# Optimization experiments

Hardware: AMD Instinct MI355X
Metric: run time of the kernel (lower is better)

The kernel has to match this reference:

```python
import jax, jax.numpy as jnp
import numpy as np

TEMPERATURE = 10.0
CE_WEIGHT = 10.0
NUM_CLUSTERS = 32  # clusters per batch element, labels in [0, K)


def setup_inputs() -> dict:
    key = jax.random.key(0)
    k1, k2, k3, k4, k5 = jax.random.split(key, 5)
    B, N, D, C, K = 4, 2048, 2, 64, NUM_CLUSTERS
    embedding = jax.random.normal(k1, (B, N, D), dtype=jnp.float32)
    contr_emb = jax.random.normal(k2, (B, N, C), dtype=jnp.float32)
    abs_coords = jax.random.normal(k3, (B, N, D), dtype=jnp.float32)
    patch_mask = jax.random.randint(k4, (B, N, N), 0, 2, dtype=jnp.int32)
    cluster_labels = jax.random.randint(k5, (B, N), 0, K, dtype=jnp.int32)
    return {
        "embedding": embedding,
        "contr_emb": contr_emb,
        "abs_coords": abs_coords,
        "patch_mask": patch_mask,
        "cluster_labels": cluster_labels,
    }


def reference(embedding, contr_emb, abs_coords, patch_mask, cluster_labels):
    B, N, D = embedding.shape
    C = contr_emb.shape[-1]
    K = NUM_CLUSTERS

    # --- anchor term: pairwise distance + nonlinearity + masked mean ---
    # diff[b,i,j,:] = (e_i - e_j) + (c_i - c_j)
    diff = (embedding[:, :, None] - embedding[:, None]) + (
        abs_coords[:, :, None] - abs_coords[:, None]
    )  # [B,N,N,D]
    dist_sq = jnp.sum(diff * diff, axis=-1)  # norm(2)^2, [B,N,N]
    nonlinear_dist = 1.0 - jnp.exp(-dist_sq / TEMPERATURE)
    m = (patch_mask == 1).astype(nonlinear_dist.dtype)
    loss = jnp.sum(nonlinear_dist * m) / jnp.sum(m)  # masked mean

    # --- contrastive term ---
    # F.normalize(contr_emb, dim=-1)
    norm = jnp.maximum(jnp.linalg.norm(contr_emb, axis=-1, keepdims=True), 1e-12)
    c = contr_emb / norm  # [B,N,C]

    # per-batch cluster means under no_grad (stop_gradient)
    onehot = jax.nn.one_hot(cluster_labels, K, dtype=c.dtype)  # [B,N,K]
    sums = jnp.einsum("bnc,bnk->bkc", c, onehot)  # [B,K,C]
    counts = jnp.maximum(jnp.sum(onehot, axis=1), 1.0)  # [B,K]
    means = jax.lax.stop_gradient(sums / counts[..., None])  # [B,K,C]

    # cat per-batch [C,K] matrices along cluster axis -> [C, B*K]
    cum_mean_clusters = means.reshape(B * K, C).T
    stacked = c.reshape(B * N, C)
    logits = stacked @ cum_mean_clusters  # [B*N, B*K]

    target = cluster_labels.reshape(-1)  # labels as written (no batch offset)
    logp = jax.nn.log_softmax(logits, axis=-1)
    nll = -jnp.take_along_axis(logp, target[:, None].astype(jnp.int32), axis=1)[:, 0]
    bce_loss = jnp.mean(nll)  # all targets >= 0, so no ignore_index hits

    return loss + CE_WEIGHT * bce_loss
```

## Files before the change

kernel.cpp:

```cpp
#include <hip/hip_runtime.h>
#include <math.h>

#define B_ 4
#define N_ 2048
#define C_ 64
#define K_ 32
#define BN_ (B_ * N_)

#define WS_NLL 0
#define WS_DONE 8
#define WS_MEANS 64
#define WS_APART 8320

__device__ __forceinline__ void pair4(float sx, float sy, float4 xs, float4 ys,
                                      int4 m, float& acc, int& cnt) {
  float dx, dy, d2, v;
  dx = sx - xs.x; dy = sy - ys.x; d2 = dx * dx + dy * dy;
  v = 1.0f - __expf(d2 * -0.1f);
  if (m.x == 1) { acc += v; cnt += 1; }
  dx = sx - xs.y; dy = sy - ys.y; d2 = dx * dx + dy * dy;
  v = 1.0f - __expf(d2 * -0.1f);
  if (m.y == 1) { acc += v; cnt += 1; }
  dx = sx - xs.z; dy = sy - ys.z; d2 = dx * dx + dy * dy;
  v = 1.0f - __expf(d2 * -0.1f);
  if (m.z == 1) { acc += v; cnt += 1; }
  dx = sx - xs.w; dy = sy - ys.w; d2 = dx * dx + dy * dy;
  v = 1.0f - __expf(d2 * -0.1f);
  if (m.w == 1) { acc += v; cnt += 1; }
}

__global__ __launch_bounds__(256) void k_main(
    const float* __restrict__ emb, const float* __restrict__ absc,
    const float* __restrict__ contr, const int* __restrict__ labels,
    const int* __restrict__ mask, float* __restrict__ ws) {
  __shared__ union {
    struct { float sx[N_]; float sy[N_]; } a;
    struct { int lab[N_]; float lsum[4][64]; float lcnt[4]; } c;
  } sm;
  __shared__ float red[8];
  int t = threadIdx.x, lane = t & 63, w = t >> 6;
  int bid = blockIdx.x;
  if (bid < 128) {
    int b = bid >> 5, k = bid & 31;
    if (bid == 0 && t == 0) {
      ws[WS_NLL] = 0.0f;
      ((unsigned*)ws)[WS_DONE] = 0u;
    }
    const int4* lab4 = (const int4*)(labels + b * N_);
    int4* l4 = (int4*)sm.c.lab;
    l4[t] = lab4[t];
    l4[t + 256] = lab4[t + 256];
    __syncthreads();
    float acc = 0.0f, cnt = 0.0f;
    for (int g0 = w * 512; g0 < w * 512 + 512; g0 += 64) {
      unsigned long long mb = __ballot(sm.c.lab[g0 + lane] == k);
      while (mb) {
        int bit = __ffsll(mb) - 1;
        mb &= mb - 1;
        int r = g0 + bit;
        float x = contr[(size_t)(b * N_ + r) * C_ + lane];
        float ss = x * x;
#pragma unroll
        for (int off = 32; off > 0; off >>= 1) ss += __shfl_xor(ss, off);
        acc += x * (1.0f / fmaxf(sqrtf(ss), 1e-12f));
        cnt += 1.0f;
      }
    }
    sm.c.lsum[w][lane] = acc;
    if (lane == 0) sm.c.lcnt[w] = cnt;
    __syncthreads();
    if (t < 64) {
      float s = sm.c.lsum[0][t] + sm.c.lsum[1][t] + sm.c.lsum[2][t] + sm.c.lsum[3][t];
      float c = sm.c.lcnt[0] + sm.c.lcnt[1] + sm.c.lcnt[2] + sm.c.lcnt[3];
      ws[WS_MEANS + (b * K_ + k) * C_ + t] = s / fmaxf(c, 1.0f);
    }
  } else {
    int aid = bid - 128;
    int b = aid >> 8;
    int flat = (aid & 255) * 256 + t;
    const float4* e4 = (const float4*)(emb + b * N_ * 2);
    const float4* a4 = (const float4*)(absc + b * N_ * 2);
    for (int i = t; i < N_ / 2; i += 256) {
      float4 ev = e4[i], av = a4[i];
      sm.a.sx[2 * i]     = ev.x + av.x;
      sm.a.sy[2 * i]     = ev.y + av.y;
      sm.a.sx[2 * i + 1] = ev.z + av.z;
      sm.a.sy[2 * i + 1] = ev.w + av.w;
    }
    __syncthreads();
    int cg = flat & 511;
    float4 xs = ((const float4*)sm.a.sx)[cg];
    float4 ys = ((const float4*)sm.a.sy)[cg];
    const int4* m4 = (const int4*)mask + (size_t)b * (N_ * (size_t)N_ / 4);
    float acc = 0.0f;
    int cnt = 0;
#pragma unroll
    for (int it = 0; it < 16; ++it) {
      int idx = flat + it * 65536;
      int4 m = m4[idx];
      int row = idx >> 9;
      pair4(sm.a.sx[row], sm.a.sy[row], xs, ys, m, acc, cnt);
    }
    float cntf = (float)cnt;
#pragma unroll
    for (int off = 32; off > 0; off >>= 1) {
      acc += __shfl_xor(acc, off);
      cntf += __shfl_xor(cntf, off);
    }
    if (lane == 0) { red[w * 2] = acc; red[w * 2 + 1] = cntf; }
    __syncthreads();
    if (t == 0) {
      ws[WS_APART + aid * 2 + 0] = red[0] + red[2] + red[4] + red[6];
      ws[WS_APART + aid * 2 + 1] = red[1] + red[3] + red[5] + red[7];
    }
  }
}

__global__ __launch_bounds__(128) void k_logits_final(
    const float* __restrict__ contr, const int* __restrict__ labels,
    float* __restrict__ ws, float* __restrict__ out) {
  __shared__ float lc[32 * C_];
  __shared__ float invr[32];
  __shared__ float lm[2][32], lsv[2][32], ltl[32];
  __shared__ float fred[4];
  __shared__ int lastf;
  int t = threadIdx.x, lane = t & 63, w = t >> 6;
  int r0 = blockIdx.x * 32;
  int j = w * 64 + lane;
  const float4* mean4 = (const float4*)(ws + WS_MEANS);
  float4 mk[16];
#pragma unroll
  for (int q = 0; q < 16; ++q) mk[q] = mean4[j * 16 + q];
  const float4* c4 = (const float4*)(contr + (size_t)r0 * C_);
  float4* lc4 = (float4*)lc;
  lc4[t] = c4[t];
  lc4[t + 128] = c4[t + 128];
  lc4[t + 256] = c4[t + 256];
  lc4[t + 384] = c4[t + 384];
  __syncthreads();
  for (int r = w * 16; r < w * 16 + 16; ++r) {
    float x = lc[r * C_ + lane];
    float ss = x * x;
#pragma unroll
    for (int off = 32; off > 0; off >>= 1) ss += __shfl_xor(ss, off);
    if (lane == 0) invr[r] = 1.0f / fmaxf(sqrtf(ss), 1e-12f);
  }
  __syncthreads();
  for (int r = 0; r < 32; ++r) {
    const float4* cr = lc4 + r * 16;
    float acc = 0.0f;
#pragma unroll
    for (int q = 0; q < 16; ++q) {
      float4 cv = cr[q];
      acc += cv.x * mk[q].x + cv.y * mk[q].y + cv.z * mk[q].z + cv.w * mk[q].w;
    }
    acc *= invr[r];
    float m = acc;
#pragma unroll
    for (int off = 32; off > 0; off >>= 1) m = fmaxf(m, __shfl_xor(m, off));
    float s = __expf(acc - m);
#pragma unroll
    for (int off = 32; off > 0; off >>= 1) s += __shfl_xor(s, off);
    int tgt = labels[r0 + r];
    float tl = __shfl(acc, tgt);
    if (lane == 0) {
      lm[w][r] = m;
      lsv[w][r] = s;
      if (w == 0) ltl[r] = tl;
    }
  }
  __syncthreads();
  if (t < 32) {
    float m0 = lm[0][t], m1 = lm[1][t];
    float mm = fmaxf(m0, m1);
    float ss = lsv[0][t] * __expf(m0 - mm) + lsv[1][t] * __expf(m1 - mm);
    float nll = (mm + __logf(ss)) - ltl[t];
#pragma unroll
    for (int off = 16; off > 0; off >>= 1) nll += __shfl_xor(nll, off);
    if (t == 0) atomicAdd(&ws[WS_NLL], nll);
  }
  __syncthreads();
  if (t == 0) {
    __threadfence();
    unsigned v = atomicAdd(&((unsigned*)ws)[WS_DONE], 1u);
    lastf = (v == 255u);
  }
  __syncthreads();
  if (lastf) {
    __threadfence();
    float a = 0.0f, c = 0.0f;
    for (int i = t; i < 1024; i += 128) {
      a += ws[WS_APART + i * 2 + 0];
      c += ws[WS_APART + i * 2 + 1];
    }
#pragma unroll
    for (int off = 32; off > 0; off >>= 1) {
      a += __shfl_xor(a, off);
      c += __shfl_xor(c, off);
    }
    if (lane == 0) { fred[w * 2] = a; fred[w * 2 + 1] = c; }
    __syncthreads();
    if (t == 0) {
      float at = fred[0] + fred[2];
      float ct = fred[1] + fred[3];
      out[0] = at / ct + 10.0f * ws[WS_NLL] * (1.0f / (float)BN_);
    }
  }
}

extern "C" void kernel_launch(void* const* d_in, const int* in_sizes, int n_in,
                              void* d_out, int out_size, void* d_ws, size_t ws_size,
                              hipStream_t stream) {
  const float* emb    = (const float*)d_in[0];
  const float* contr  = (const float*)d_in[1];
  const float* absc   = (const float*)d_in[2];
  const int*   mask   = (const int*)d_in[3];
  const int*   labels = (const int*)d_in[4];
  float* ws  = (float*)d_ws;
  float* out = (float*)d_out;

  k_main<<<128 + 1024, 256, 0, stream>>>(emb, absc, contr, labels, mask, ws);
  k_logits_final<<<256, 128, 0, stream>>>(contr, labels, ws, out);
}
```

Baseline: 154.8 us.

## Drop max-subtraction in softmax, halve rows per block, batch dot products

The logits kernel now handles 16 rows per block across 512 blocks instead of 32 rows across 256. The softmax max reduction is removed, which is safe because the logits are cosine-like values with magnitude at most about 1. The 16 dot products are computed first and their shuffle reductions run afterwards, and each row norm is computed by a single thread instead of a wave shuffle. This shortens the serial dependency chain and spreads the work over more blocks. In exchange, each block reloads the mean vectors, so twice as much mean data is read in total.

```diff
diff --git a/kernel.cpp b/kernel.cpp
--- a/kernel.cpp
+++ b/kernel.cpp
@@ -119,13 +119,13 @@
 __global__ __launch_bounds__(128) void k_logits_final(
     const float* __restrict__ contr, const int* __restrict__ labels,
     float* __restrict__ ws, float* __restrict__ out) {
-  __shared__ float lc[32 * C_];
-  __shared__ float invr[32];
-  __shared__ float lm[2][32], lsv[2][32], ltl[32];
+  __shared__ float lc[16 * C_];
+  __shared__ float invr[16];
+  __shared__ float lsv[2][16], ltl[16];
   __shared__ float fred[4];
   __shared__ int lastf;
   int t = threadIdx.x, lane = t & 63, w = t >> 6;
-  int r0 = blockIdx.x * 32;
+  int r0 = blockIdx.x * 16;
   int j = w * 64 + lane;
   const float4* mean4 = (const float4*)(ws + WS_MEANS);
   float4 mk[16];
@@ -135,55 +135,54 @@
   float4* lc4 = (float4*)lc;
   lc4[t] = c4[t];
   lc4[t + 128] = c4[t + 128];
-  lc4[t + 256] = c4[t + 256];
-  lc4[t + 384] = c4[t + 384];
-  __syncthreads();
-  for (int r = w * 16; r < w * 16 + 16; ++r) {
-    float x = lc[r * C_ + lane];
-    float ss = x * x;
-#pragma unroll
-    for (int off = 32; off > 0; off >>= 1) ss += __shfl_xor(ss, off);
-    if (lane == 0) invr[r] = 1.0f / fmaxf(sqrtf(ss), 1e-12f);
-  }
-  __syncthreads();
-  for (int r = 0; r < 32; ++r) {
+  __syncthreads();
+  if (t < 16) {
+    float ss = 0.0f;
+#pragma unroll
+    for (int q = 0; q < 16; ++q) {
+      float4 v = lc4[t * 16 + q];
+      ss += v.x * v.x + v.y * v.y + v.z * v.z + v.w * v.w;
+    }
+    invr[t] = 1.0f / fmaxf(sqrtf(ss), 1e-12f);
+  }
+  __syncthreads();
+  float acc[16];
+#pragma unroll
+  for (int r = 0; r < 16; ++r) {
     const float4* cr = lc4 + r * 16;
-    float acc = 0.0f;
+    float a = 0.0f;
 #pragma unroll
     for (int q = 0; q < 16; ++q) {
       float4 cv = cr[q];
-      acc += cv.x * mk[q].x + cv.y * mk[q].y + cv.z * mk[q].z + cv.w * mk[q].w;
-    }
-    acc *= invr[r];
-    float m = acc;
-#pragma unroll
-    for (int off = 32; off > 0; off >>= 1) m = fmaxf(m, __shfl_xor(m, off));
-    float s = __expf(acc - m);
+      a += cv.x * mk[q].x + cv.y * mk[q].y + cv.z * mk[q].z + cv.w * mk[q].w;
+    }
+    acc[r] = a;
+  }
+#pragma unroll
+  for (int r = 0; r < 16; ++r) {
+    float l = acc[r] * invr[r];
+    float s = __expf(l);
 #pragma unroll
     for (int off = 32; off > 0; off >>= 1) s += __shfl_xor(s, off);
     int tgt = labels[r0 + r];
-    float tl = __shfl(acc, tgt);
+    float tl = __shfl(l, tgt);
     if (lane == 0) {
-      lm[w][r] = m;
       lsv[w][r] = s;
       if (w == 0) ltl[r] = tl;
     }
   }
   __syncthreads();
-  if (t < 32) {
-    float m0 = lm[0][t], m1 = lm[1][t];
-    float mm = fmaxf(m0, m1);
-    float ss = lsv[0][t] * __expf(m0 - mm) + lsv[1][t] * __expf(m1 - mm);
-    float nll = (mm + __logf(ss)) - ltl[t];
-#pragma unroll
-    for (int off = 16; off > 0; off >>= 1) nll += __shfl_xor(nll, off);
+  if (t < 16) {
+    float nll = __logf(lsv[0][t] + lsv[1][t]) - ltl[t];
+#pragma unroll
+    for (int off = 8; off > 0; off >>= 1) nll += __shfl_xor(nll, off);
     if (t == 0) atomicAdd(&ws[WS_NLL], nll);
   }
   __syncthreads();
   if (t == 0) {
     __threadfence();
     unsigned v = atomicAdd(&((unsigned*)ws)[WS_DONE], 1u);
-    lastf = (v == 255u);
+    lastf = (v == 511u);
   }
   __syncthreads();
   if (lastf) {
@@ -220,5 +219,5 @@
   float* out = (float*)d_out;
 
   k_main<<<128 + 1024, 256, 0, stream>>>(emb, absc, contr, labels, mask, ws);
-  k_logits_final<<<256, 128, 0, stream>>>(contr, labels, ws, out);
-}
+  k_logits_final<<<512, 128, 0, stream>>>(contr, labels, ws, out);
+}
```

After: 196.5 us. 1.27x slower.
